# Kernel tuning notes

Hardware: AMD Instinct MI355X
Metric: run time of the kernel (lower is better)

## Reference

```python
import jax, jax.numpy as jnp
import numpy as np

H = 2048        # hidden_size
NH = 16         # num_heads
NOPE = 128      # qk_nope_head_dim
ROPE = 64       # qk_rope_head_dim
VD = 128        # v_head_dim
QLORA = 1536    # q_lora_rank
KVLORA = 512    # kv_lora_rank
THETA = 1000000.0
EPS = 1e-6
B, S = 2, 2048


def _rope_cos_sin(position_ids):
    # inv_freq over even dims, emb = cat(freqs, freqs); indexed by position_ids
    inv_freq = 1.0 / (THETA ** (jnp.arange(0, ROPE, 2, dtype=jnp.float32) / ROPE))
    freqs = position_ids.astype(jnp.float32)[..., None] * inv_freq  # [b,s,ROPE/2]
    emb = jnp.concatenate([freqs, freqs], axis=-1)                  # [b,s,ROPE]
    # unsqueeze_dim=1 -> broadcast over heads
    return jnp.cos(emb)[:, None], jnp.sin(emb)[:, None]             # [b,1,s,ROPE]


def _apply_rope(x, cos, sin):
    # torch: view(b,h,s,d//2,2).transpose(4,3).reshape -> interleaved-to-half-split permutation
    xp = jnp.concatenate([x[..., 0::2], x[..., 1::2]], axis=-1)
    x1, x2 = jnp.split(xp, 2, axis=-1)
    rot = jnp.concatenate([-x2, x1], axis=-1)  # rotate_half
    return xp * cos + rot * sin


def setup_inputs() -> dict:
    key = jax.random.key(0)
    ks = jax.random.split(key, 7)
    s = 0.02
    hidden_states = jax.random.normal(ks[0], (B, S, H), jnp.float32)
    position_ids = jnp.broadcast_to(jnp.arange(S, dtype=jnp.int64 if jax.config.jax_enable_x64 else jnp.int32), (B, S))
    attention_mask = jnp.broadcast_to(jnp.tril(jnp.ones((S, S), bool))[None, None], (B, 1, S, S))
    Wq_down = jax.random.normal(ks[1], (QLORA, H), jnp.float32) * s
    q_ln_w = jnp.ones((QLORA,), jnp.float32)
    Wq_up = jax.random.normal(ks[2], (NH * (NOPE + ROPE), QLORA), jnp.float32) * s
    Wkv_down = jax.random.normal(ks[3], (KVLORA + ROPE, H), jnp.float32) * s
    Wkv_up = jax.random.normal(ks[4], (NH * (NOPE + VD), KVLORA), jnp.float32) * s
    Wo = jax.random.normal(ks[5], (H, NH * VD), jnp.float32) * s
    return {
        'hidden_states': hidden_states, 'position_ids': position_ids,
        'attention_mask': attention_mask, 'Wq_down': Wq_down, 'q_ln_w': q_ln_w,
        'Wq_up': Wq_up, 'Wkv_down': Wkv_down, 'Wkv_up': Wkv_up, 'Wo': Wo,
    }


def reference(hidden_states, position_ids, attention_mask,
              Wq_down, q_ln_w, Wq_up, Wkv_down, Wkv_up, Wo):
    b, s, _ = hidden_states.shape
    dtype = hidden_states.dtype

    # --- Q path: down-proj -> RMSNorm -> up-proj ---
    ql = hidden_states @ Wq_down.T                                   # [b,s,QLORA]
    var = jnp.mean(jnp.square(ql.astype(jnp.float32)), -1, keepdims=True)
    ql = (q_ln_w * (ql.astype(jnp.float32) * jax.lax.rsqrt(var + EPS)).astype(dtype))
    q = (ql @ Wq_up.T).reshape(b, s, NH, NOPE + ROPE).transpose(0, 2, 1, 3)  # [b,h,s,d]
    q_nope, q_rope = q[..., :NOPE], q[..., NOPE:]

    cos, sin = _rope_cos_sin(position_ids)                           # [b,1,s,ROPE]
    q_rope = _apply_rope(q_rope, cos, sin)                           # [b,h,s,ROPE]

    # --- KV path: single down-proj, split into compressed_kv and rope part ---
    ckv = hidden_states @ Wkv_down.T                                 # [b,s,KVLORA+ROPE]
    compressed_kv, k_rope = ckv[..., :KVLORA], ckv[..., KVLORA:]
    k_rope = _apply_rope(k_rope[:, None], cos, sin)[:, 0]            # [b,s,ROPE]
    # NOTE: kv_down_layernorm is declared in __init__ but never applied in forward.

    # --- absorption trick: fold kv_up into q / output ---
    kv_up = Wkv_up.reshape(NH, NOPE + VD, KVLORA)
    q_absorb = kv_up[:, :NOPE, :]                                    # [h,NOPE,KVLORA]
    out_absorb = kv_up[:, NOPE:, :]                                  # [h,VD,KVLORA]
    q_abs = jnp.einsum('bhsn,hnc->bhsc', q_nope, q_absorb)           # [b,h,s,KVLORA]

    scale = 1.0 / np.sqrt(NOPE + ROPE)
    scores = (jnp.einsum('bhqr,bkr->bhqk', q_rope, k_rope)
              + jnp.einsum('bhqc,bkc->bhqk', q_abs, compressed_kv)) * scale
    scores = jnp.where(attention_mask, scores, -jnp.inf)
    attn = jax.nn.softmax(scores.astype(jnp.float32), axis=-1).astype(dtype)

    out = jnp.einsum('bhqk,bkc->bhqc', attn, compressed_kv)          # [b,h,s,KVLORA]
    out = jnp.einsum('bhqc,hvc->bhqv', out, out_absorb)              # [b,h,s,VD]
    out = out.transpose(0, 2, 1, 3).reshape(b, s, NH * VD)
    return out @ Wo.T                                                # [b,s,H]
```

## Files before the change

kernel.cpp:

```cpp
#include <hip/hip_runtime.h>
#include <cstdint>

#define S_LEN 2048
#define NH_N  16

typedef short s16x8 __attribute__((ext_vector_type(8)));
typedef unsigned short u16x8 __attribute__((ext_vector_type(8)));
typedef float f32x4 __attribute__((ext_vector_type(4)));

__device__ __forceinline__ float b2f(unsigned short u) {
    return __uint_as_float(((uint32_t)u) << 16);
}
__device__ __forceinline__ unsigned short f2b(float f) {
    uint32_t x = __float_as_uint(f);
    x += 0x7fffu + ((x >> 16) & 1u);
    return (unsigned short)(x >> 16);
}

__device__ __forceinline__ void cstore(unsigned short* p, float v) { *p = f2b(v); }
__device__ __forceinline__ void cstore(float* p, float v) { *p = v; }

__device__ __forceinline__ void gl2lds16(const void* g, void* l) {
    __builtin_amdgcn_global_load_lds(
        (const __attribute__((address_space(1))) unsigned int*)g,
        (__attribute__((address_space(3))) unsigned int*)l, 16, 0, 0);
}

__global__ __launch_bounds__(256) void f32_to_bf16(const float* __restrict__ in,
                                                   unsigned short* __restrict__ out,
                                                   long n)
{
    const long nv = n >> 2;
    long i = (long)blockIdx.x * blockDim.x + threadIdx.x;
    const long stride = (long)gridDim.x * blockDim.x;
    for (; i < nv; i += stride) {
        float4 v = ((const float4*)in)[i];
        ushort4 o;
        o.x = f2b(v.x); o.y = f2b(v.y); o.z = f2b(v.z); o.w = f2b(v.w);
        ((ushort4*)out)[i] = o;
    }
}

template <typename CT>
__global__ __launch_bounds__(256) void gemm128(
    const unsigned short* __restrict__ A, const unsigned short* __restrict__ B,
    CT* __restrict__ C,
    int K, int lda, int ldb, int ldc, int Nlim,
    long sAb, long sAh, long sBb, long sBh, long sCb, long sCh)
{
    __shared__ unsigned short Alds[128 * 32];
    __shared__ unsigned short Blds[128 * 32];
    const int z = blockIdx.z, b = z >> 4, h = z & 15;
    A += (long)b * sAb + (long)h * sAh;
    B += (long)b * sBb + (long)h * sBh;
    C += (long)b * sCb + (long)h * sCh;
    const int tid = threadIdx.x;
    const int lane = tid & 63, w = tid >> 6;
    const int l15 = lane & 15, q4 = lane >> 4;
    const int m0 = blockIdx.x * 128, n0 = blockIdx.y * 128;
    const int wm = (w >> 1) * 64, wn = (w & 1) * 64;

    int srow[2], sgc[2];
#pragma unroll
    for (int it = 0; it < 2; ++it) {
        const int g = it * 256 + tid;
        const int row = g >> 2, gp = g & 3;
        srow[it] = row;
        sgc[it] = gp ^ ((row ^ (row >> 2)) & 3);
    }
    int aoff[4], boff[4];
#pragma unroll
    for (int i = 0; i < 4; ++i) {
        const int ra = wm + i * 16 + l15;
        aoff[i] = ra * 32 + (q4 ^ ((ra ^ (ra >> 2)) & 3)) * 8;
        const int rb = wn + i * 16 + l15;
        boff[i] = rb * 32 + (q4 ^ ((rb ^ (rb >> 2)) & 3)) * 8;
    }

    f32x4 acc[4][4];
#pragma unroll
    for (int i = 0; i < 4; ++i)
#pragma unroll
        for (int j = 0; j < 4; ++j) acc[i][j] = (f32x4){0.f, 0.f, 0.f, 0.f};

    for (int k0 = 0; k0 < K; k0 += 32) {
        __syncthreads();
#pragma unroll
        for (int it = 0; it < 2; ++it) {
            gl2lds16(A + (long)(m0 + srow[it]) * lda + k0 + sgc[it] * 8,
                     (char*)Alds + ((it * 256 + w * 64) << 4));
            gl2lds16(B + (long)(n0 + srow[it]) * ldb + k0 + sgc[it] * 8,
                     (char*)Blds + ((it * 256 + w * 64) << 4));
        }
        __syncthreads();
        s16x8 af[4], bf[4];
#pragma unroll
        for (int i = 0; i < 4; ++i) {
            af[i] = *(const s16x8*)(Alds + aoff[i]);
            bf[i] = *(const s16x8*)(Blds + boff[i]);
        }
#pragma unroll
        for (int i = 0; i < 4; ++i)
#pragma unroll
            for (int j = 0; j < 4; ++j)
                acc[i][j] = __builtin_amdgcn_mfma_f32_16x16x32_bf16(af[i], bf[j], acc[i][j], 0, 0, 0);
    }

#pragma unroll
    for (int i = 0; i < 4; ++i) {
        const int row0 = m0 + wm + i * 16 + q4 * 4;
#pragma unroll
        for (int j = 0; j < 4; ++j) {
            const int col = n0 + wn + j * 16 + l15;
            if (col < Nlim) {
#pragma unroll
                for (int r = 0; r < 4; ++r)
                    cstore(&C[(long)(row0 + r) * ldc + col], acc[i][j][r]);
            }
        }
    }
}

__global__ __launch_bounds__(256) void rmsnorm_k(unsigned short* __restrict__ ql,
                                                 const unsigned short* __restrict__ w)
{
    const long base = (long)blockIdx.x * 1536;
    const int tid = threadIdx.x;
    float v[6];
    float ss = 0.f;
#pragma unroll
    for (int i = 0; i < 6; ++i) {
        v[i] = b2f(ql[base + tid + i * 256]);
        ss += v[i] * v[i];
    }
#pragma unroll
    for (int off = 32; off; off >>= 1) ss += __shfl_xor(ss, off, 64);
    __shared__ float red[4];
    if ((tid & 63) == 0) red[tid >> 6] = ss;
    __syncthreads();
    const float tot = red[0] + red[1] + red[2] + red[3];
    const float r = rsqrtf(tot * (1.0f / 1536.0f) + 1e-6f);
#pragma unroll
    for (int i = 0; i < 6; ++i) {
        const int idx = tid + i * 256;
        ql[base + idx] = f2b(v[i] * r * b2f(w[idx]));
    }
}

__global__ __launch_bounds__(512) void rope_k(
    const unsigned short* __restrict__ q, const unsigned short* __restrict__ ckv,
    const int* __restrict__ pos_ids,
    unsigned short* __restrict__ q_rope, unsigned short* __restrict__ krope)
{
    const int bs = blockIdx.x;
    const int b = bs >> 11, s = bs & 2047;
    const int t = threadIdx.x;
    const int j = t & 31, h = t >> 5;
    const float pos = (float)pos_ids[bs];
    const float invf = __expf(-(float)j * 0.4317347f);
    float sn, cs;
    sincosf(pos * invf, &sn, &cs);
    const unsigned short* x = q + (long)bs * 3072 + h * 192 + 128;
    const float x0 = b2f(x[2 * j]), x1 = b2f(x[2 * j + 1]);
    const long ob = ((long)(b * NH_N + h) * S_LEN + s) * 64;
    q_rope[ob + j]      = f2b(x0 * cs - x1 * sn);
    q_rope[ob + 32 + j] = f2b(x1 * cs + x0 * sn);
    if (h == 0) {
        const unsigned short* y = ckv + (long)bs * 576 + 512;
        const float y0 = b2f(y[2 * j]), y1 = b2f(y[2 * j + 1]);
        const long ob2 = (long)bs * 64;
        krope[ob2 + j]      = f2b(y0 * cs - y1 * sn);
        krope[ob2 + 32 + j] = f2b(y1 * cs + y0 * sn);
    }
}

__global__ __launch_bounds__(256) void transpose_qabsorb(
    const unsigned short* __restrict__ Wkv_up, unsigned short* __restrict__ qT)
{
    const int idx = blockIdx.x * 256 + threadIdx.x;
    const int n = idx & 127;
    const int c = (idx >> 7) & 511;
    const int h = idx >> 16;
    qT[idx] = Wkv_up[((long)(h * 256 + n)) * 512 + c];
}

__global__ __launch_bounds__(256) void transpose_ckv(
    const unsigned short* __restrict__ ckv, unsigned short* __restrict__ VT_g)
{
    __shared__ unsigned short t[64][72];
    const int k0 = blockIdx.x * 64, c0 = blockIdx.y * 64, b = blockIdx.z;
    const int tid = threadIdx.x;
#pragma unroll
    for (int it = 0; it < 2; ++it) {
        int idx = tid + it * 256;
        int row = idx >> 3, g = idx & 7;
        *(s16x8*)&t[row][g * 8] =
            *(const s16x8*)(ckv + ((long)(b * S_LEN + k0 + row) * 576 + c0 + g * 8));
    }
    __syncthreads();
#pragma unroll
    for (int it = 0; it < 2; ++it) {
        int idx = tid + it * 256;
        int c = idx >> 3, g = idx & 7;
        u16x8 v;
#pragma unroll
        for (int j = 0; j < 8; ++j) v[j] = t[g * 8 + j][c];
        *(u16x8*)(VT_g + ((long)(b * 512 + c0 + c) * S_LEN + k0 + g * 8)) = v;
    }
}

__global__ __launch_bounds__(512, 1) void flash_mfma(
    const unsigned short* __restrict__ qabs,  const unsigned short* __restrict__ qrope,
    const unsigned short* __restrict__ ckv,   const unsigned short* __restrict__ krope,
    const unsigned short* __restrict__ VT_g,  unsigned short* __restrict__ attn_out)
{
    __shared__ unsigned short K_lds[2][2304 * 8];
    __shared__ unsigned short VT_lds[2][2048 * 8];
    __shared__ unsigned short P_lds[8][16 * 40];

    const float scale = 0.07216878364870323f;
    const int tid = threadIdx.x;
    const int lane = tid & 63, w = tid >> 6;
    const int l15 = lane & 15, q4 = lane >> 4;
    const int bh = blockIdx.x;
    const int b = bh >> 4;

    const unsigned short* ckv_b  = ckv   + (long)b * S_LEN * 576;
    const unsigned short* krop_b = krope + (long)b * S_LEN * 64;
    const unsigned short* vt_b   = VT_g  + (long)b * 512 * S_LEN;

    int koff[4], voff[4];
#pragma unroll
    for (int it = 0; it < 4; ++it) {
        const int idx = it * 512 + tid;
        const int key = ((idx >> 6) & 1) * 16 + (idx & 15);
        const int g   = (idx >> 7) * 4 + ((idx >> 4) & 3);
        koff[it] = key * 576 + g * 8;
        const int c   = (idx >> 6) * 16 + (idx & 15);
        voff[it] = c * S_LEN + ((idx >> 4) & 3) * 8;
    }
    const int hoff = (((tid >> 6) & 1) * 16 + (tid & 15)) * 64 +
                     ((tid >> 7) * 4 + ((tid >> 4) & 3)) * 8;

#pragma unroll 1
    for (int half = 0; half < 2; ++half) {
        const int qt = half ? blockIdx.y : 15 - blockIdx.y;
        const int q0 = qt * 128;

        s16x8 qf[18];
        {
            const unsigned short* qa = qabs + ((long)bh * S_LEN + q0 + w * 16 + l15) * 512 + q4 * 8;
#pragma unroll
            for (int kb = 0; kb < 16; ++kb) qf[kb] = *(const s16x8*)(qa + kb * 32);
            const unsigned short* qr = qrope + ((long)bh * S_LEN + q0 + w * 16 + l15) * 64 + q4 * 8;
            qf[16] = *(const s16x8*)(qr);
            qf[17] = *(const s16x8*)(qr + 32);
        }

        f32x4 O[32];
#pragma unroll
        for (int nb = 0; nb < 32; ++nb) O[nb] = (f32x4){0.f, 0.f, 0.f, 0.f};
        float m_i[4] = {-INFINITY, -INFINITY, -INFINITY, -INFINITY};
        float l_i[4] = {0.f, 0.f, 0.f, 0.f};

        const int nkt = 4 * qt + 4;
        unsigned short *Kc = K_lds[0], *Kn = K_lds[1];
        unsigned short *Vc = VT_lds[0], *Vn = VT_lds[1];

        {
#pragma unroll
            for (int it = 0; it < 4; ++it)
                gl2lds16(ckv_b + koff[it], (char*)Kc + ((it * 512 + w * 64) << 4));
            if (tid < 256)
                gl2lds16(krop_b + hoff, (char*)Kc + ((2048 + w * 64) << 4));
#pragma unroll
            for (int it = 0; it < 4; ++it)
                gl2lds16(vt_b + voff[it], (char*)Vc + ((it * 512 + w * 64) << 4));
        }
        __syncthreads();

        for (int kt = 0; kt < nkt; ++kt) {
            const int k0 = kt * 32;

            if (kt + 1 < nkt) {
                const int kn = k0 + 32;
                const unsigned short* cs = ckv_b + (long)kn * 576;
#pragma unroll
                for (int it = 0; it < 4; ++it)
                    gl2lds16(cs + koff[it], (char*)Kn + ((it * 512 + w * 64) << 4));
                if (tid < 256)
                    gl2lds16(krop_b + (long)kn * 64 + hoff, (char*)Kn + ((2048 + w * 64) << 4));
                const unsigned short* vs = vt_b + kn;
#pragma unroll
                for (int it = 0; it < 4; ++it)
                    gl2lds16(vs + voff[it], (char*)Vn + ((it * 512 + w * 64) << 4));
            }

            if (k0 <= q0 + (w << 4) + 15) {
                f32x4 s0 = {0.f, 0.f, 0.f, 0.f}, s1 = s0;
#pragma unroll
                for (int kb = 0; kb < 18; ++kb) {
                    s16x8 k0f = *(const s16x8*)&Kc[((kb * 2 + 0) * 64 + lane) * 8];
                    s16x8 k1f = *(const s16x8*)&Kc[((kb * 2 + 1) * 64 + lane) * 8];
                    s0 = __builtin_amdgcn_mfma_f32_16x16x32_bf16(qf[kb], k0f, s0, 0, 0, 0);
                    s1 = __builtin_amdgcn_mfma_f32_16x16x32_bf16(qf[kb], k1f, s1, 0, 0, 0);
                }
#pragma unroll
                for (int r = 0; r < 4; ++r) { s0[r] *= scale; s1[r] *= scale; }
                if (k0 + 31 > q0 + (w << 4)) {
#pragma unroll
                    for (int r = 0; r < 4; ++r) {
                        const int qg = q0 + w * 16 + q4 * 4 + r;
                        if (k0 + l15 > qg)      s0[r] = -INFINITY;
                        if (k0 + 16 + l15 > qg) s1[r] = -INFINITY;
                    }
                }

                float al[4];
#pragma unroll
                for (int r = 0; r < 4; ++r) {
                    float mx = fmaxf(s0[r], s1[r]);
#pragma unroll
                    for (int off = 1; off < 16; off <<= 1) mx = fmaxf(mx, __shfl_xor(mx, off, 64));
                    const float mn = fmaxf(m_i[r], mx);
                    al[r] = __expf(m_i[r] - mn);
                    m_i[r] = mn;
                    const float p0 = __expf(s0[r] - mn);
                    const float p1 = __expf(s1[r] - mn);
                    float ps = p0 + p1;
#pragma unroll
                    for (int off = 1; off < 16; off <<= 1) ps += __shfl_xor(ps, off, 64);
                    l_i[r] = l_i[r] * al[r] + ps;
                    P_lds[w][(q4 * 4 + r) * 40 + l15]      = f2b(p0);
                    P_lds[w][(q4 * 4 + r) * 40 + 16 + l15] = f2b(p1);
                }

                const float alm = al[0] * al[1] * al[2] * al[3];
                if (__any(alm != 1.0f)) {
#pragma unroll
                    for (int nb = 0; nb < 32; ++nb)
#pragma unroll
                        for (int r = 0; r < 4; ++r) O[nb][r] *= al[r];
                }

                s16x8 pf = *(const s16x8*)&P_lds[w][l15 * 40 + q4 * 8];
#pragma unroll
                for (int nb = 0; nb < 32; ++nb) {
                    s16x8 vf = *(const s16x8*)&Vc[(nb * 64 + lane) * 8];
                    O[nb] = __builtin_amdgcn_mfma_f32_16x16x32_bf16(pf, vf, O[nb], 0, 0, 0);
                }
            }

            __syncthreads();
            unsigned short* t;
            t = Kc; Kc = Kn; Kn = t;
            t = Vc; Vc = Vn; Vn = t;
        }

        float inv[4];
#pragma unroll
        for (int r = 0; r < 4; ++r) inv[r] = 1.0f / l_i[r];
#pragma unroll
        for (int r = 0; r < 4; ++r) {
            const long rowbase = ((long)bh * S_LEN + q0 + w * 16 + q4 * 4 + r) * 512;
#pragma unroll
            for (int nb = 0; nb < 32; ++nb)
                attn_out[rowbase + nb * 16 + l15] = f2b(O[nb][r] * inv[r]);
        }
    }
}

extern "C" void kernel_launch(void* const* d_in, const int* in_sizes, int n_in,
                              void* d_out, int out_size, void* d_ws, size_t ws_size,
                              hipStream_t stream)
{
    (void)in_sizes; (void)n_in; (void)out_size; (void)ws_size;
    const float* hs_f       = (const float*)d_in[0];
    const int*   pos        = (const int*)d_in[1];
    const float* Wq_down_f  = (const float*)d_in[3];
    const float* q_ln_w_f   = (const float*)d_in[4];
    const float* Wq_up_f    = (const float*)d_in[5];
    const float* Wkv_down_f = (const float*)d_in[6];
    const float* Wkv_up_f   = (const float*)d_in[7];
    const float* Wo_f       = (const float*)d_in[8];
    float* out = (float*)d_out;

    unsigned short* ws    = (unsigned short*)d_ws;
    unsigned short* ql    = ws;
    unsigned short* q     = ql    + 4096L * 1536;
    unsigned short* out2  = q;
    unsigned short* ckv   = q     + 4096L * 3072;
    unsigned short* krope = ckv   + 4096L * 576;
    unsigned short* qrope = krope + 4096L * 64;
    unsigned short* qabsT = qrope + 32L * 2048 * 64;
    unsigned short* qabs  = qabsT + 16L * 512 * 128;
    unsigned short* attno = qabs  + 32L * 2048 * 512;
    unsigned short* hs    = attno + 32L * 2048 * 512;
    unsigned short* Wqd   = hs    + 4096L * 2048;
    unsigned short* qlnw  = Wqd   + 1536L * 2048;
    unsigned short* Wqu   = qlnw  + 1536;
    unsigned short* Wkvd  = Wqu   + 3072L * 1536;
    unsigned short* Wkvu  = Wkvd  + 576L * 2048;
    unsigned short* Wob   = Wkvu  + 16L * 256 * 512;
    unsigned short* VTg   = Wob   + 2048L * 2048;

    f32_to_bf16<<<4096, 256, 0, stream>>>(hs_f,       hs,   4096L * 2048);
    f32_to_bf16<<<3072, 256, 0, stream>>>(Wq_down_f,  Wqd,  1536L * 2048);
    f32_to_bf16<<<2,    256, 0, stream>>>(q_ln_w_f,   qlnw, 1536L);
    f32_to_bf16<<<4096, 256, 0, stream>>>(Wq_up_f,    Wqu,  3072L * 1536);
    f32_to_bf16<<<1152, 256, 0, stream>>>(Wkv_down_f, Wkvd, 576L * 2048);
    f32_to_bf16<<<2048, 256, 0, stream>>>(Wkv_up_f,   Wkvu, 16L * 256 * 512);
    f32_to_bf16<<<4096, 256, 0, stream>>>(Wo_f,       Wob,  2048L * 2048);

    gemm128<unsigned short><<<dim3(32, 12, 1), 256, 0, stream>>>(hs, Wqd, ql,
        2048, 2048, 2048, 1536, 1536, 0, 0, 0, 0, 0, 0);
    rmsnorm_k<<<4096, 256, 0, stream>>>(ql, qlnw);
    gemm128<unsigned short><<<dim3(32, 24, 1), 256, 0, stream>>>(ql, Wqu, q,
        1536, 1536, 1536, 3072, 3072, 0, 0, 0, 0, 0, 0);
    gemm128<unsigned short><<<dim3(32, 5, 1), 256, 0, stream>>>(hs, Wkvd, ckv,
        2048, 2048, 2048, 576, 576, 0, 0, 0, 0, 0, 0);
    rope_k<<<4096, 512, 0, stream>>>(q, ckv, pos, qrope, krope);
    transpose_ckv<<<dim3(32, 8, 2), 256, 0, stream>>>(ckv, VTg);
    transpose_qabsorb<<<4096, 256, 0, stream>>>(Wkvu, qabsT);
    gemm128<unsigned short><<<dim3(16, 4, 32), 256, 0, stream>>>(q, qabsT, qabs,
        128, 3072, 128, 512, 512,
        2048L * 3072, 192, 0, 512L * 128, 16L * 2048 * 512, 2048L * 512);
    flash_mfma<<<dim3(32, 8, 1), 512, 0, stream>>>(qabs, qrope, ckv, krope, VTg, attno);
    gemm128<unsigned short><<<dim3(16, 1, 32), 256, 0, stream>>>(attno, Wkvu + 128L * 512, out2,
        512, 512, 512, 2048, 128,
        16L * 2048 * 512, 2048L * 512, 0, 256L * 512, 2048L * 2048, 128);
    gemm128<float><<<dim3(32, 16, 1), 256, 0, stream>>>(out2, Wob, out,
        2048, 2048, 2048, 2048, 2048, 0, 0, 0, 0, 0, 0);
}
```

Measured before the change: 796.3 us.

## Load V fragments directly from global with padded stride, defer row-sum reduction

Drops the LDS double-buffer for the transposed V tile and has each wave load its V MFMA operands straight from global memory, using a padded leading dimension (2080) to avoid channel/bank conflicts. Moves the per-tile cross-lane row-sum shuffle reduction of the softmax denominator to a single reduction at the end. Adds s_setprio around the MFMA blocks. This frees LDS and removes per-tile LDS traffic, but V is now re-read from global/L2 by every wave rather than shared through LDS. It also relies on the workspace being large enough for the padded VT layout.

```diff
diff --git a/kernel.cpp b/kernel.cpp
--- a/kernel.cpp
+++ b/kernel.cpp
@@ -3,6 +3,7 @@
 
 #define S_LEN 2048
 #define NH_N  16
+#define VT_LD 2080
 
 typedef short s16x8 __attribute__((ext_vector_type(8)));
 typedef unsigned short u16x8 __attribute__((ext_vector_type(8)));
@@ -205,7 +206,7 @@
         u16x8 v;
 #pragma unroll
         for (int j = 0; j < 8; ++j) v[j] = t[g * 8 + j][c];
-        *(u16x8*)(VT_g + ((long)(b * 512 + c0 + c) * S_LEN + k0 + g * 8)) = v;
+        *(u16x8*)(VT_g + ((long)(b * 512 + c0 + c) * VT_LD + k0 + g * 8)) = v;
     }
 }
 
@@ -215,7 +216,6 @@
     const unsigned short* __restrict__ VT_g,  unsigned short* __restrict__ attn_out)
 {
     __shared__ unsigned short K_lds[2][2304 * 8];
-    __shared__ unsigned short VT_lds[2][2048 * 8];
     __shared__ unsigned short P_lds[8][16 * 40];
 
     const float scale = 0.07216878364870323f;
@@ -227,20 +227,20 @@
 
     const unsigned short* ckv_b  = ckv   + (long)b * S_LEN * 576;
     const unsigned short* krop_b = krope + (long)b * S_LEN * 64;
-    const unsigned short* vt_b   = VT_g  + (long)b * 512 * S_LEN;
-
-    int koff[4], voff[4];
+    const unsigned short* vt_b   = VT_g  + (long)b * 512 * VT_LD;
+
+    int koff[4];
 #pragma unroll
     for (int it = 0; it < 4; ++it) {
         const int idx = it * 512 + tid;
         const int key = ((idx >> 6) & 1) * 16 + (idx & 15);
         const int g   = (idx >> 7) * 4 + ((idx >> 4) & 3);
         koff[it] = key * 576 + g * 8;
-        const int c   = (idx >> 6) * 16 + (idx & 15);
-        voff[it] = c * S_LEN + ((idx >> 4) & 3) * 8;
     }
     const int hoff = (((tid >> 6) & 1) * 16 + (tid & 15)) * 64 +
                      ((tid >> 7) * 4 + ((tid >> 4) & 3)) * 8;
+
+    const long vbase = (long)l15 * VT_LD + q4 * 8;
 
 #pragma unroll 1
     for (int half = 0; half < 2; ++half) {
@@ -265,7 +265,6 @@
 
         const int nkt = 4 * qt + 4;
         unsigned short *Kc = K_lds[0], *Kn = K_lds[1];
-        unsigned short *Vc = VT_lds[0], *Vn = VT_lds[1];
 
         {
 #pragma unroll
@@ -273,9 +272,6 @@
                 gl2lds16(ckv_b + koff[it], (char*)Kc + ((it * 512 + w * 64) << 4));
             if (tid < 256)
                 gl2lds16(krop_b + hoff, (char*)Kc + ((2048 + w * 64) << 4));
-#pragma unroll
-            for (int it = 0; it < 4; ++it)
-                gl2lds16(vt_b + voff[it], (char*)Vc + ((it * 512 + w * 64) << 4));
         }
         __syncthreads();
 
@@ -290,14 +286,11 @@
                     gl2lds16(cs + koff[it], (char*)Kn + ((it * 512 + w * 64) << 4));
                 if (tid < 256)
                     gl2lds16(krop_b + (long)kn * 64 + hoff, (char*)Kn + ((2048 + w * 64) << 4));
-                const unsigned short* vs = vt_b + kn;
-#pragma unroll
-                for (int it = 0; it < 4; ++it)
-                    gl2lds16(vs + voff[it], (char*)Vn + ((it * 512 + w * 64) << 4));
             }
 
             if (k0 <= q0 + (w << 4) + 15) {
                 f32x4 s0 = {0.f, 0.f, 0.f, 0.f}, s1 = s0;
+                __builtin_amdgcn_s_setprio(1);
 #pragma unroll
                 for (int kb = 0; kb < 18; ++kb) {
                     s16x8 k0f = *(const s16x8*)&Kc[((kb * 2 + 0) * 64 + lane) * 8];
@@ -305,6 +298,7 @@
                     s0 = __builtin_amdgcn_mfma_f32_16x16x32_bf16(qf[kb], k0f, s0, 0, 0, 0);
                     s1 = __builtin_amdgcn_mfma_f32_16x16x32_bf16(qf[kb], k1f, s1, 0, 0, 0);
                 }
+                __builtin_amdgcn_s_setprio(0);
 #pragma unroll
                 for (int r = 0; r < 4; ++r) { s0[r] *= scale; s1[r] *= scale; }
                 if (k0 + 31 > q0 + (w << 4)) {
@@ -327,10 +321,7 @@
                     m_i[r] = mn;
                     const float p0 = __expf(s0[r] - mn);
                     const float p1 = __expf(s1[r] - mn);
-                    float ps = p0 + p1;
-#pragma unroll
-                    for (int off = 1; off < 16; off <<= 1) ps += __shfl_xor(ps, off, 64);
-                    l_i[r] = l_i[r] * al[r] + ps;
+                    l_i[r] = l_i[r] * al[r] + (p0 + p1);
                     P_lds[w][(q4 * 4 + r) * 40 + l15]      = f2b(p0);
                     P_lds[w][(q4 * 4 + r) * 40 + 16 + l15] = f2b(p1);
                 }
@@ -344,22 +335,34 @@
                 }
 
                 s16x8 pf = *(const s16x8*)&P_lds[w][l15 * 40 + q4 * 8];
-#pragma unroll
-                for (int nb = 0; nb < 32; ++nb) {
-                    s16x8 vf = *(const s16x8*)&Vc[(nb * 64 + lane) * 8];
-                    O[nb] = __builtin_amdgcn_mfma_f32_16x16x32_bf16(pf, vf, O[nb], 0, 0, 0);
+                const unsigned short* vp = vt_b + vbase + k0;
+#pragma unroll
+                for (int g = 0; g < 4; ++g) {
+                    s16x8 vf[8];
+#pragma unroll
+                    for (int j = 0; j < 8; ++j)
+                        vf[j] = *(const s16x8*)(vp + (long)(g * 8 + j) * (16 * VT_LD));
+                    __builtin_amdgcn_s_setprio(1);
+#pragma unroll
+                    for (int j = 0; j < 8; ++j)
+                        O[g * 8 + j] = __builtin_amdgcn_mfma_f32_16x16x32_bf16(pf, vf[j], O[g * 8 + j], 0, 0, 0);
+                    __builtin_amdgcn_s_setprio(0);
                 }
             }
 
             __syncthreads();
             unsigned short* t;
             t = Kc; Kc = Kn; Kn = t;
-            t = Vc; Vc = Vn; Vn = t;
         }
 
         float inv[4];
 #pragma unroll
-        for (int r = 0; r < 4; ++r) inv[r] = 1.0f / l_i[r];
+        for (int r = 0; r < 4; ++r) {
+            float ls = l_i[r];
+#pragma unroll
+            for (int off = 1; off < 16; off <<= 1) ls += __shfl_xor(ls, off, 64);
+            inv[r] = 1.0f / ls;
+        }
 #pragma unroll
         for (int r = 0; r < 4; ++r) {
             const long rowbase = ((long)bh * S_LEN + q0 + w * 16 + q4 * 4 + r) * 512;
```

After: 993.0 us. 1.25x slower.
